# Performance work log

Hardware: AMD Instinct MI355X
Metric: run time of the kernel (lower is better)

The kernel has to match this reference:

```python
import jax, jax.numpy as jnp
import numpy as np

N, D_IN, D, E, B = 30000, 512, 512, 300000, 4096
N_RES, N_DNN = 2, 2
EPS = 1e-5


def _ln(x, g, b):
    mu = jnp.mean(x, axis=-1, keepdims=True)
    var = jnp.mean((x - mu) ** 2, axis=-1, keepdims=True)
    return (x - mu) * jax.lax.rsqrt(var + EPS) * g + b


def setup_inputs() -> dict:
    key = jax.random.key(0)
    ks = jax.random.split(key, 16)
    s = 1.0 / np.sqrt(D)
    inp = {
        "node_feat": jax.random.normal(ks[0], (N, D_IN), jnp.float32),
        "edge_hop0": jax.random.randint(ks[1], (2, E), 0, N, jnp.int32),
        "edge_hop1": jax.random.randint(ks[2], (2, E), 0, N, jnp.int32),
        "target_idx": jax.random.randint(ks[3], (B,), 0, N, jnp.int32),
        # node transform
        "Wt": jax.random.normal(ks[4], (D_IN, D), jnp.float32) / np.sqrt(D_IN),
        "bt": jnp.zeros((D,), jnp.float32),
        # GATConv (shared across both hops, one relation)
        "Wf": jax.random.normal(ks[5], (D, D), jnp.float32) * s,
        "bf": jnp.zeros((D,), jnp.float32),
        "w_att": jax.random.normal(ks[6], (2 * D,), jnp.float32) * s,
        "b_att": jnp.zeros((), jnp.float32),
        "gat_bias": jnp.zeros((D,), jnp.float32),
        # Res_DNN
        "Wp": jax.random.normal(ks[7], (D, D), jnp.float32) * s,
        "bp": jnp.zeros((D,), jnp.float32),
        "dnn_W": jax.random.normal(ks[8], (N_RES, N_DNN, D, D), jnp.float32) * s,
        "dnn_b": jnp.zeros((N_RES, N_DNN, D), jnp.float32),
        "dnn_g": jnp.ones((N_RES, N_DNN, D), jnp.float32),
        "dnn_beta": jnp.zeros((N_RES, N_DNN, D), jnp.float32),
        "res_g": jnp.ones((N_RES, D), jnp.float32),
        "res_beta": jnp.zeros((N_RES, D), jnp.float32),
        "Wc": jax.random.normal(ks[9], (D, 1), jnp.float32) * s,
        "bc": jnp.zeros((1,), jnp.float32),
    }
    return inp


def _gat(feat, edges, Wf, bf, w_att, b_att, gat_bias):
    # dst and src are the same node set / same features here
    h = feat @ Wf + bf                      # [N, D]
    di, si = edges[0], edges[1]             # [E], [E]
    # att(concat(dst_h, src_h)) == dst_h @ w[:D] + src_h @ w[D:] + b
    sd = h @ w_att[:D]                      # [N]
    ss = h @ w_att[D:]                      # [N]
    e = jnp.tanh(sd[di] + ss[si] + b_att)   # [E]
    # sparse softmax per destination row
    m = jax.ops.segment_max(e, di, num_segments=N)
    a = jnp.exp(e - m[di])
    denom = jax.ops.segment_sum(a, di, num_segments=N)
    alpha = a / denom[di]                   # [E]
    # sparse-mm aggregation
    out = jax.ops.segment_sum(alpha[:, None] * h[si], di, num_segments=N)
    return out + gat_bias


def reference(node_feat, edge_hop0, edge_hop1, target_idx, Wt, bt, Wf, bf,
              w_att, b_att, gat_bias, Wp, bp, dnn_W, dnn_b, dnn_g, dnn_beta,
              res_g, res_beta, Wc, bc):
    # node-type feature transform (dropout is identity at inference)
    feat = node_feat @ Wt + bt              # [N, D]
    # hops processed from last to first: hop1 then hop0
    for edges in (edge_hop1, edge_hop0):
        g = _gat(feat, edges, Wf, bf, w_att, b_att, gat_bias)
        feat = (feat + g) * 0.5             # mean of stacked [orig, gat_out]
    h = feat[target_idx]                    # [B, D]
    # Res_DNN head
    h = h @ Wp + bp
    for r in range(N_RES):
        sc = h
        for i in range(N_DNN):
            h = _ln(jnp.tanh(h @ dnn_W[r, i] + dnn_b[r, i]), dnn_g[r, i], dnn_beta[r, i])
        h = _ln(jnp.tanh(sc + h), res_g[r], res_beta[r])
    logits = h @ Wc + bc                    # [B, 1]
    return jax.nn.sigmoid(logits)
```

## Files before the change

### kernel.cpp

```cpp
#include <hip/hip_runtime.h>

#define D 512
typedef unsigned short ushort_t;
typedef __attribute__((ext_vector_type(8))) short bf16x8;
typedef __attribute__((ext_vector_type(4))) float f32x4;

static __device__ __forceinline__ ushort_t f2bf(float f) {
  unsigned u = __float_as_uint(f);
  u += 0x7fffu + ((u >> 16) & 1u);
  return (ushort_t)(u >> 16);
}
static __device__ __forceinline__ float bf2f(ushort_t h) {
  return __uint_as_float(((unsigned)h) << 16);
}

static __device__ __forceinline__ void gld_lds16(const void* g, void* lds) {
  __builtin_amdgcn_global_load_lds(
      (const __attribute__((address_space(1))) unsigned int*)g,
      (__attribute__((address_space(3))) unsigned int*)lds, 16, 0, 0);
}

__global__ __launch_bounds__(256) void pack_weight(
    const float* __restrict__ W, ushort_t* __restrict__ out, int K, int N, int nmat) {
  int i = blockIdx.x * 256 + threadIdx.x;
  const int per = K * N;
  if (i >= per * nmat) return;
  const int mat = i / per;
  const int r = i - mat * per;
  const int k = r / N, n = r - k * N;
  const int nt = n >> 4, col = n & 15, kt = k >> 5, kg = (k >> 3) & 3, j = k & 7;
  out[(size_t)mat * per + (((size_t)nt * (K >> 5) + kt) << 9) + ((kg << 4) + col) * 8 + j] =
      f2bf(W[(size_t)mat * per + r]);
}

__global__ __launch_bounds__(256) void conv_bf16_pad(
    const float* __restrict__ in, ushort_t* __restrict__ out, int M, int Mp, int K) {
  const size_t i4 = ((size_t)blockIdx.x * 256 + threadIdx.x) * 4;
  if (i4 >= (size_t)Mp * K) return;
  const int row = (int)(i4 / K);
  ushort4 o;
  if (row < M) {
    const float4 v = *reinterpret_cast<const float4*>(&in[i4]);
    o.x = f2bf(v.x); o.y = f2bf(v.y); o.z = f2bf(v.z); o.w = f2bf(v.w);
  } else {
    o.x = o.y = o.z = o.w = 0;
  }
  *reinterpret_cast<ushort4*>(&out[i4]) = o;
}

__global__ __launch_bounds__(256) void gemm_mfma(
    const ushort_t* __restrict__ A, const ushort_t* __restrict__ Bp,
    const float* __restrict__ bias, ushort_t* __restrict__ C16, int N, int K) {
  __shared__ __align__(16) ushort_t As[8 * 512];
  __shared__ __align__(16) ushort_t Bs[8 * 512];
  const int nwg = gridDim.x;
  const int q = nwg >> 3, rm = nwg & 7;
  const int xcd = blockIdx.x & 7, kk = blockIdx.x >> 3;
  const int lin = (xcd < rm ? xcd * (q + 1) : rm * (q + 1) + (xcd - rm) * q) + kk;
  const int m0 = (lin >> 2) * 128;
  const int n0 = (lin & 3) * 128;
  const int tid = threadIdx.x;
  const int lane = tid & 63;
  const int wid = tid >> 6;
  const int wm = wid >> 1, wn = wid & 1;
  const int arow = lane & 15;
  const int akoff = (lane >> 4) * 8;
  const int kt32 = K >> 5;
  f32x4 acc[4][4] = {};
  ushort_t* as0 = &As[(wid * 2 + 0) * 512];
  ushort_t* as1 = &As[(wid * 2 + 1) * 512];
  ushort_t* bs0 = &Bs[(wid * 2 + 0) * 512];
  ushort_t* bs1 = &Bs[(wid * 2 + 1) * 512];
  for (int k0 = 0; k0 < K; k0 += 32) {
    gld_lds16(&A[(size_t)(m0 + (wid * 2 + 0) * 16 + arow) * K + k0 + akoff], as0);
    gld_lds16(&A[(size_t)(m0 + (wid * 2 + 1) * 16 + arow) * K + k0 + akoff], as1);
    gld_lds16(&Bp[(((size_t)(n0 / 16 + wid * 2 + 0) * kt32 + (k0 >> 5)) << 9) + lane * 8], bs0);
    gld_lds16(&Bp[(((size_t)(n0 / 16 + wid * 2 + 1) * kt32 + (k0 >> 5)) << 9) + lane * 8], bs1);
    __syncthreads();
    bf16x8 af[4], bfr[4];
#pragma unroll
    for (int mi = 0; mi < 4; ++mi)
      af[mi] = *reinterpret_cast<const bf16x8*>(&As[(wm * 4 + mi) * 512 + lane * 8]);
#pragma unroll
    for (int ni = 0; ni < 4; ++ni)
      bfr[ni] = *reinterpret_cast<const bf16x8*>(&Bs[(wn * 4 + ni) * 512 + lane * 8]);
#pragma unroll
    for (int mi = 0; mi < 4; ++mi)
#pragma unroll
      for (int ni = 0; ni < 4; ++ni)
        acc[mi][ni] = __builtin_amdgcn_mfma_f32_16x16x32_bf16(af[mi], bfr[ni], acc[mi][ni], 0, 0, 0);
    __syncthreads();
  }
#pragma unroll
  for (int mi = 0; mi < 4; ++mi) {
    const int row = m0 + wm * 64 + mi * 16 + ((lane >> 4) << 2);
#pragma unroll
    for (int ni = 0; ni < 4; ++ni) {
      const int col = n0 + wn * 64 + ni * 16 + (lane & 15);
      const float bv = bias[col];
#pragma unroll
      for (int r = 0; r < 4; ++r)
        C16[(size_t)(row + r) * N + col] = f2bf(acc[mi][ni][r] + bv);
    }
  }
}

__global__ __launch_bounds__(256) void rowdot2_w(
    const ushort_t* __restrict__ hb, const float* __restrict__ w_att,
    float* __restrict__ sd, float* __restrict__ ss, int Nn) {
  const int r = blockIdx.x * 4 + (threadIdx.x >> 6);
  const int lane = threadIdx.x & 63;
  if (r >= Nn) return;
  const bf16x8 hv = *reinterpret_cast<const bf16x8*>(&hb[(size_t)r * D + lane * 8]);
  float d0 = 0.f, d1 = 0.f;
#pragma unroll
  for (int q = 0; q < 8; ++q) {
    const float v = bf2f((ushort_t)hv[q]);
    d0 += v * w_att[lane * 8 + q];
    d1 += v * w_att[D + lane * 8 + q];
  }
#pragma unroll
  for (int off = 32; off > 0; off >>= 1) {
    d0 += __shfl_xor(d0, off);
    d1 += __shfl_xor(d1, off);
  }
  if (lane == 0) { sd[r] = d0; ss[r] = d1; }
}

__global__ void count_deg2(const int* __restrict__ e1, const int* __restrict__ e0,
                           int* __restrict__ deg, int Nn, int E) {
  const int e = blockIdx.x * blockDim.x + threadIdx.x;
  if (e < E) {
    atomicAdd(&deg[e1[e]], 1);
    atomicAdd(&deg[Nn + e0[e]], 1);
  }
}

__global__ __launch_bounds__(256) void scan_block(
    const int* __restrict__ deg, int* __restrict__ incl, int* __restrict__ bsum, int n) {
  __shared__ int buf[256];
  const int t = threadIdx.x;
  const int i = blockIdx.x * 256 + t;
  const int v = (i < n) ? deg[i] : 0;
  buf[t] = v;
  __syncthreads();
  for (int off = 1; off < 256; off <<= 1) {
    const int y = (t >= off) ? buf[t - off] : 0;
    __syncthreads();
    buf[t] += y;
    __syncthreads();
  }
  if (i < n) incl[i] = buf[t];
  if (t == 255) bsum[blockIdx.x] = buf[255];
}

__global__ __launch_bounds__(256) void scan_sums(
    int* __restrict__ bsum, int nb, int* __restrict__ row_total) {
  __shared__ int buf[256];
  const int t = threadIdx.x;
  const int v = (t < nb) ? bsum[t] : 0;
  buf[t] = v;
  __syncthreads();
  for (int off = 1; off < 256; off <<= 1) {
    const int y = (t >= off) ? buf[t - off] : 0;
    __syncthreads();
    buf[t] += y;
    __syncthreads();
  }
  if (t < nb) bsum[t] = buf[t] - v;
  if (t == 0) *row_total = buf[255];
}

__global__ __launch_bounds__(256) void scan_finalize(
    const int* __restrict__ incl, const int* __restrict__ deg,
    const int* __restrict__ bsum, int* __restrict__ row_start,
    int* __restrict__ cursor, int n) {
  const int i = blockIdx.x * 256 + threadIdx.x;
  if (i >= n) return;
  const int v = incl[i] - deg[i] + bsum[i >> 8];
  row_start[i] = v;
  cursor[i] = v;
}

__global__ void fill_csr2(const int* __restrict__ e1, const int* __restrict__ e0,
                          int* __restrict__ cursor, int* __restrict__ csr_s,
                          int Nn, int E) {
  const int e = blockIdx.x * blockDim.x + threadIdx.x;
  if (e >= E) return;
  const int d1 = e1[e];
  csr_s[atomicAdd(&cursor[d1], 1)] = e1[E + e];
  const int d0 = e0[e];
  csr_s[atomicAdd(&cursor[Nn + d0], 1)] = e0[E + e];
}

__global__ __launch_bounds__(256) void gat_aggregate_w(
    ushort_t* __restrict__ featb, const ushort_t* __restrict__ hb,
    const float* __restrict__ sd, const float* __restrict__ ss,
    float* __restrict__ edge_e, const float* __restrict__ b_att_p,
    const float* __restrict__ gat_bias, const int* __restrict__ row_start,
    const int* __restrict__ csr_src, int Nn) {
  const int dst = blockIdx.x * 4 + (threadIdx.x >> 6);
  const int lane = threadIdx.x & 63;
  if (dst >= Nn) return;
  const int beg = row_start[dst];
  const int end = row_start[dst + 1];
  const int deg = end - beg;
  const float sdd = sd[dst];
  const float ba = b_att_p[0];
  float acc[8] = {};
  float inv;
  if (deg <= 64) {
    const int j0 = beg + lane;
    const bool valid = j0 < end;
    const float e = valid ? tanhf(sdd + ss[csr_src[j0]] + ba) : -1e30f;
    float m = e;
#pragma unroll
    for (int off = 32; off > 0; off >>= 1) m = fmaxf(m, __shfl_xor(m, off));
    float a = valid ? expf(e - m) : 0.f;
    float s = a;
#pragma unroll
    for (int off = 32; off > 0; off >>= 1) s += __shfl_xor(s, off);
    inv = (s > 0.f) ? 1.f / s : 0.f;
    int k = 0;
    for (; k + 1 < deg; k += 2) {
      const float w0 = __shfl(a, k) * inv;
      const float w1 = __shfl(a, k + 1) * inv;
      const int s0 = csr_src[beg + k];
      const int s1 = csr_src[beg + k + 1];
      const bf16x8 h0 = *reinterpret_cast<const bf16x8*>(&hb[(size_t)s0 * D + lane * 8]);
      const bf16x8 h1 = *reinterpret_cast<const bf16x8*>(&hb[(size_t)s1 * D + lane * 8]);
#pragma unroll
      for (int q = 0; q < 8; ++q)
        acc[q] += w0 * bf2f((ushort_t)h0[q]) + w1 * bf2f((ushort_t)h1[q]);
    }
    if (k < deg) {
      const float w = __shfl(a, k) * inv;
      const int s0 = csr_src[beg + k];
      const bf16x8 h0 = *reinterpret_cast<const bf16x8*>(&hb[(size_t)s0 * D + lane * 8]);
#pragma unroll
      for (int q = 0; q < 8; ++q) acc[q] += w * bf2f((ushort_t)h0[q]);
    }
  } else {
    float m = -1e30f;
    for (int j = beg + lane; j < end; j += 64) {
      const float e = tanhf(sdd + ss[csr_src[j]] + ba);
      edge_e[j] = e;
      m = fmaxf(m, e);
    }
#pragma unroll
    for (int off = 32; off > 0; off >>= 1) m = fmaxf(m, __shfl_xor(m, off));
    asm volatile("s_waitcnt vmcnt(0)" ::: "memory");
    float s = 0.f;
    for (int j = beg + lane; j < end; j += 64) {
      const float a2 = expf(edge_e[j] - m);
      edge_e[j] = a2;
      s += a2;
    }
#pragma unroll
    for (int off = 32; off > 0; off >>= 1) s += __shfl_xor(s, off);
    asm volatile("s_waitcnt vmcnt(0)" ::: "memory");
    inv = (s > 0.f) ? 1.f / s : 0.f;
    for (int j = beg; j < end; ++j) {
      const float w = edge_e[j] * inv;
      const int sidx = csr_src[j];
      const bf16x8 hv = *reinterpret_cast<const bf16x8*>(&hb[(size_t)sidx * D + lane * 8]);
#pragma unroll
      for (int q = 0; q < 8; ++q) acc[q] += w * bf2f((ushort_t)hv[q]);
    }
  }
  const size_t o = (size_t)dst * D + lane * 8;
  bf16x8 fv = *reinterpret_cast<const bf16x8*>(&featb[o]);
#pragma unroll
  for (int q = 0; q < 8; ++q) {
    const float f = (bf2f((ushort_t)fv[q]) + acc[q] + gat_bias[lane * 8 + q]) * 0.5f;
    fv[q] = (short)f2bf(f);
  }
  *reinterpret_cast<bf16x8*>(&featb[o]) = fv;
}

__global__ __launch_bounds__(1024, 4) void head_fused(
    const ushort_t* __restrict__ featb, const int* __restrict__ tidx,
    const ushort_t* __restrict__ pWp, const float* __restrict__ bp,
    const ushort_t* __restrict__ pDW, const float* __restrict__ dnn_b,
    const float* __restrict__ dnn_g, const float* __restrict__ dnn_be,
    const float* __restrict__ res_g, const float* __restrict__ res_be,
    const float* __restrict__ Wc, const float* __restrict__ bc,
    float* __restrict__ out) {
  __shared__ __align__(16) ushort_t A_lds[16 * 512];
  __shared__ float lsum[16][16], lsq[16][16], meanv[16], rsv[16];
  const int tid = threadIdx.x;
  const int lane = tid & 63;
  const int wave = tid >> 6;
  const int nt0 = wave * 2;
  const int c15 = lane & 15;
  const int rgrp = lane >> 4;

  {
    const int row = tid >> 6, col8 = tid & 63;
    const int g = tidx[blockIdx.x * 16 + row];
    const bf16x8 v = *reinterpret_cast<const bf16x8*>(&featb[(size_t)g * D + col8 * 8]);
    *reinterpret_cast<bf16x8*>(&A_lds[row * 512 + (col8 ^ (row & 7)) * 8]) = v;
  }
  __syncthreads();

  auto do_gemm = [&](const ushort_t* __restrict__ W, f32x4& a0, f32x4& a1) {
    a0 = f32x4{0.f, 0.f, 0.f, 0.f};
    a1 = f32x4{0.f, 0.f, 0.f, 0.f};
    bf16x8 c0 = *reinterpret_cast<const bf16x8*>(
        &W[(((size_t)nt0 * 16 + 0) << 9) + lane * 8]);
    bf16x8 c1 = *reinterpret_cast<const bf16x8*>(
        &W[(((size_t)(nt0 + 1) * 16 + 0) << 9) + lane * 8]);
#pragma unroll
    for (int kt = 0; kt < 16; ++kt) {
      bf16x8 n0 = c0, n1 = c1;
      if (kt < 15) {
        n0 = *reinterpret_cast<const bf16x8*>(
            &W[(((size_t)nt0 * 16 + kt + 1) << 9) + lane * 8]);
        n1 = *reinterpret_cast<const bf16x8*>(
            &W[(((size_t)(nt0 + 1) * 16 + kt + 1) << 9) + lane * 8]);
      }
      const int col8 = kt * 4 + rgrp;
      const bf16x8 af = *reinterpret_cast<const bf16x8*>(
          &A_lds[c15 * 512 + (col8 ^ (c15 & 7)) * 8]);
      a0 = __builtin_amdgcn_mfma_f32_16x16x32_bf16(af, c0, a0, 0, 0, 0);
      a1 = __builtin_amdgcn_mfma_f32_16x16x32_bf16(af, c1, a1, 0, 0, 0);
      c0 = n0;
      c1 = n1;
    }
  };

  auto block_ln = [&](f32x4& v0, f32x4& v1, const float* __restrict__ g,
                      const float* __restrict__ be) {
    float psum[4], psq[4];
#pragma unroll
    for (int r = 0; r < 4; ++r) {
      psum[r] = v0[r] + v1[r];
      psq[r] = v0[r] * v0[r] + v1[r] * v1[r];
    }
#pragma unroll
    for (int off = 8; off > 0; off >>= 1)
#pragma unroll
      for (int r = 0; r < 4; ++r) {
        psum[r] += __shfl_xor(psum[r], off);
        psq[r] += __shfl_xor(psq[r], off);
      }
    if (c15 == 0) {
#pragma unroll
      for (int r = 0; r < 4; ++r) {
        lsum[wave][rgrp * 4 + r] = psum[r];
        lsq[wave][rgrp * 4 + r] = psq[r];
      }
    }
    __syncthreads();
    if (tid < 16) {
      float s = 0.f, qq = 0.f;
#pragma unroll
      for (int w = 0; w < 16; ++w) { s += lsum[w][tid]; qq += lsq[w][tid]; }
      const float mean = s * (1.f / 512.f);
      const float var = qq * (1.f / 512.f) - mean * mean;
      meanv[tid] = mean;
      rsv[tid] = rsqrtf(var + 1e-5f);
    }
    __syncthreads();
    const int col0 = nt0 * 16 + c15;
    const int col1 = (nt0 + 1) * 16 + c15;
    const float g0 = g[col0], b0 = be[col0];
    const float g1 = g[col1], b1 = be[col1];
#pragma unroll
    for (int r = 0; r < 4; ++r) {
      const int row = rgrp * 4 + r;
      v0[r] = (v0[r] - meanv[row]) * rsv[row] * g0 + b0;
      v1[r] = (v1[r] - meanv[row]) * rsv[row] * g1 + b1;
    }
  };

  auto store_A = [&](const f32x4& v0, const f32x4& v1) {
    const int col0 = nt0 * 16 + c15;
    const int col1 = (nt0 + 1) * 16 + c15;
#pragma unroll
    for (int r = 0; r < 4; ++r) {
      const int row = rgrp * 4 + r;
      A_lds[row * 512 + (((col0 >> 3) ^ (row & 7)) << 3) + (col0 & 7)] = f2bf(v0[r]);
      A_lds[row * 512 + (((col1 >> 3) ^ (row & 7)) << 3) + (col1 & 7)] = f2bf(v1[r]);
    }
  };

  f32x4 sc0, sc1, acc0, acc1, ln0, ln1;

  do_gemm(pWp, acc0, acc1);
  {
    const float bv0 = bp[nt0 * 16 + c15];
    const float bv1 = bp[(nt0 + 1) * 16 + c15];
#pragma unroll
    for (int r = 0; r < 4; ++r) { sc0[r] = acc0[r] + bv0; sc1[r] = acc1[r] + bv1; }
  }
  __syncthreads();
  store_A(sc0, sc1);
  __syncthreads();

  for (int rb = 0; rb < 2; ++rb) {
    {
      const int st = rb * 2;
      do_gemm(pDW + (size_t)st * D * D, acc0, acc1);
      const float bv0 = dnn_b[st * D + nt0 * 16 + c15];
      const float bv1 = dnn_b[st * D + (nt0 + 1) * 16 + c15];
#pragma unroll
      for (int r = 0; r < 4; ++r) {
        acc0[r] = tanhf(acc0[r] + bv0);
        acc1[r] = tanhf(acc1[r] + bv1);
      }
      block_ln(acc0, acc1, dnn_g + st * D, dnn_be + st * D);
      store_A(acc0, acc1);
      __syncthreads();
    }
    {
      const int st = rb * 2 + 1;
      do_gemm(pDW + (size_t)st * D * D, ln0, ln1);
      const float bv0 = dnn_b[st * D + nt0 * 16 + c15];
      const float bv1 = dnn_b[st * D + (nt0 + 1) * 16 + c15];
#pragma unroll
      for (int r = 0; r < 4; ++r) {
        ln0[r] = tanhf(ln0[r] + bv0);
        ln1[r] = tanhf(ln1[r] + bv1);
      }
      block_ln(ln0, ln1, dnn_g + st * D, dnn_be + st * D);
    }
#pragma unroll
    for (int r = 0; r < 4; ++r) {
      acc0[r] = tanhf(sc0[r] + ln0[r]);
      acc1[r] = tanhf(sc1[r] + ln1[r]);
    }
    block_ln(acc0, acc1, res_g + rb * D, res_be + rb * D);
    sc0 = acc0;
    sc1 = acc1;
    if (rb == 0) {
      store_A(sc0, sc1);
      __syncthreads();
    }
  }

  float pr[4];
  {
    const float w0 = Wc[nt0 * 16 + c15];
    const float w1 = Wc[(nt0 + 1) * 16 + c15];
#pragma unroll
    for (int r = 0; r < 4; ++r) pr[r] = sc0[r] * w0 + sc1[r] * w1;
  }
#pragma unroll
  for (int off = 8; off > 0; off >>= 1)
#pragma unroll
    for (int r = 0; r < 4; ++r) pr[r] += __shfl_xor(pr[r], off);
  __syncthreads();
  if (c15 == 0) {
#pragma unroll
    for (int r = 0; r < 4; ++r) lsum[wave][rgrp * 4 + r] = pr[r];
  }
  __syncthreads();
  if (tid < 16) {
    float s = 0.f;
#pragma unroll
    for (int w = 0; w < 16; ++w) s += lsum[w][tid];
    out[blockIdx.x * 16 + tid] = 1.f / (1.f + expf(-(s + bc[0])));
  }
}

extern "C" void kernel_launch(void* const* d_in, const int* in_sizes, int n_in,
                              void* d_out, int out_size, void* d_ws, size_t ws_size,
                              hipStream_t stream) {
  (void)n_in; (void)out_size; (void)ws_size;
  const float* node_feat = (const float*)d_in[0];
  const int* edge0 = (const int*)d_in[1];
  const int* edge1 = (const int*)d_in[2];
  const int* tidx = (const int*)d_in[3];
  const float* Wt = (const float*)d_in[4];
  const float* bt = (const float*)d_in[5];
  const float* Wf = (const float*)d_in[6];
  const float* bfp = (const float*)d_in[7];
  const float* w_att = (const float*)d_in[8];
  const float* b_att = (const float*)d_in[9];
  const float* gat_bias = (const float*)d_in[10];
  const float* Wp = (const float*)d_in[11];
  const float* bp = (const float*)d_in[12];
  const float* dnn_W = (const float*)d_in[13];
  const float* dnn_b = (const float*)d_in[14];
  const float* dnn_g = (const float*)d_in[15];
  const float* dnn_be = (const float*)d_in[16];
  const float* res_g = (const float*)d_in[17];
  const float* res_be = (const float*)d_in[18];
  const float* Wc = (const float*)d_in[19];
  const float* bc = (const float*)d_in[20];
  float* out = (float*)d_out;

  const int Nn = in_sizes[0] / D;
  const int E = in_sizes[1] / 2;
  const int B = in_sizes[3];
  const int K_IN = in_sizes[4] / D;
  const int Mp = (Nn + 127) / 128 * 128;
  const int N2 = 2 * Nn;

  char* p = (char*)d_ws;
  auto alloc = [&](size_t bytes) -> char* {
    char* r = p;
    p += (bytes + 255) & ~(size_t)255;
    return r;
  };
  ushort_t* featb = (ushort_t*)alloc((size_t)Mp * D * 2);
  ushort_t* hb = (ushort_t*)alloc((size_t)Mp * D * 2);
  float* sd = (float*)alloc((size_t)Nn * 4);
  float* ss = (float*)alloc((size_t)Nn * 4);
  int* deg = (int*)alloc((size_t)N2 * 4);
  int* incl = (int*)alloc((size_t)N2 * 4);
  int* bsum = (int*)alloc(256 * 4);
  int* cursor = (int*)alloc((size_t)N2 * 4);
  int* row_start = (int*)alloc((size_t)(N2 + 1) * 4);
  int* csr_s = (int*)alloc((size_t)2 * E * 4);
  float* edge_e = (float*)alloc((size_t)2 * E * 4);
  ushort_t* pWt = (ushort_t*)alloc((size_t)K_IN * D * 2);
  ushort_t* pWf = (ushort_t*)alloc((size_t)D * D * 2);
  ushort_t* pWp = (ushort_t*)alloc((size_t)D * D * 2);
  ushort_t* pDWall = (ushort_t*)alloc((size_t)4 * D * D * 2);

  dim3 blk(256);
  const int nb2 = (N2 + 255) / 256;
  const int nw4 = (Nn + 3) / 4;

  {
    pack_weight<<<(K_IN * D + 255) / 256, blk, 0, stream>>>(Wt, pWt, K_IN, D, 1);
    pack_weight<<<(D * D + 255) / 256, blk, 0, stream>>>(Wf, pWf, D, D, 1);
    pack_weight<<<(D * D + 255) / 256, blk, 0, stream>>>(Wp, pWp, D, D, 1);
    pack_weight<<<(4 * D * D + 255) / 256, blk, 0, stream>>>(dnn_W, pDWall, D, D, 4);
    conv_bf16_pad<<<((size_t)Mp * K_IN / 4 + 255) / 256, blk, 0, stream>>>(
        node_feat, hb , Nn, Mp, K_IN);
  }

  hipMemsetAsync(deg, 0, (size_t)N2 * 4, stream);
  count_deg2<<<(E + 255) / 256, blk, 0, stream>>>(edge1, edge0, deg, Nn, E);
  scan_block<<<nb2, blk, 0, stream>>>(deg, incl, bsum, N2);
  scan_sums<<<1, blk, 0, stream>>>(bsum, nb2, &row_start[N2]);
  scan_finalize<<<nb2, blk, 0, stream>>>(incl, deg, bsum, row_start, cursor, N2);
  fill_csr2<<<(E + 255) / 256, blk, 0, stream>>>(edge1, edge0, cursor, csr_s, Nn, E);

  gemm_mfma<<<dim3(4 * (Mp / 128)), blk, 0, stream>>>(hb, pWt, bt, featb, D, K_IN);

  for (int hp = 0; hp < 2; ++hp) {
    gemm_mfma<<<dim3(4 * (Mp / 128)), blk, 0, stream>>>(featb, pWf, bfp, hb, D, D);
    rowdot2_w<<<nw4, blk, 0, stream>>>(hb, w_att, sd, ss, Nn);
    gat_aggregate_w<<<nw4, blk, 0, stream>>>(featb, hb, sd, ss, edge_e, b_att,
                                             gat_bias, row_start + hp * Nn, csr_s, Nn);
  }

  head_fused<<<B / 16, dim3(1024), 0, stream>>>(
      featb, tidx, pWp, bp, pDWall, dnn_b, dnn_g, dnn_be, res_g, res_be,
      Wc, bc, out);
}
```

Measured before the change: 357.8 us.

## Double-buffer GEMM LDS tiles and unroll GAT gather with shuffled indices

The GEMM now double-buffers its A/B LDS tiles, issuing the next k-slice's global-to-LDS loads before the MFMAs on the current slice. This drops one barrier per iteration and overlaps load latency with compute. The GAT aggregation for small-degree rows now broadcasts source indices and pre-normalized weights via lane shuffles instead of re-reading csr_src, unrolls the gather by four to keep more row loads in flight, and hoists the feature load to the top of the kernel. These add LDS usage and register pressure, which may lower occupancy.

After: 355.4 us. About the same (-0.7%).

```diff
diff --git a/kernel.cpp b/kernel.cpp
--- a/kernel.cpp
+++ b/kernel.cpp
@@ -51,8 +51,8 @@
 __global__ __launch_bounds__(256) void gemm_mfma(
     const ushort_t* __restrict__ A, const ushort_t* __restrict__ Bp,
     const float* __restrict__ bias, ushort_t* __restrict__ C16, int N, int K) {
-  __shared__ __align__(16) ushort_t As[8 * 512];
-  __shared__ __align__(16) ushort_t Bs[8 * 512];
+  __shared__ __align__(16) ushort_t As[2][8 * 512];
+  __shared__ __align__(16) ushort_t Bs[2][8 * 512];
   const int nwg = gridDim.x;
   const int q = nwg >> 3, rm = nwg & 7;
   const int xcd = blockIdx.x & 7, kk = blockIdx.x >> 3;
@@ -67,29 +67,38 @@
   const int akoff = (lane >> 4) * 8;
   const int kt32 = K >> 5;
   f32x4 acc[4][4] = {};
-  ushort_t* as0 = &As[(wid * 2 + 0) * 512];
-  ushort_t* as1 = &As[(wid * 2 + 1) * 512];
-  ushort_t* bs0 = &Bs[(wid * 2 + 0) * 512];
-  ushort_t* bs1 = &Bs[(wid * 2 + 1) * 512];
-  for (int k0 = 0; k0 < K; k0 += 32) {
-    gld_lds16(&A[(size_t)(m0 + (wid * 2 + 0) * 16 + arow) * K + k0 + akoff], as0);
-    gld_lds16(&A[(size_t)(m0 + (wid * 2 + 1) * 16 + arow) * K + k0 + akoff], as1);
-    gld_lds16(&Bp[(((size_t)(n0 / 16 + wid * 2 + 0) * kt32 + (k0 >> 5)) << 9) + lane * 8], bs0);
-    gld_lds16(&Bp[(((size_t)(n0 / 16 + wid * 2 + 1) * kt32 + (k0 >> 5)) << 9) + lane * 8], bs1);
-    __syncthreads();
+
+  auto stage = [&](int kt, int b) {
+    const int k0 = kt * 32;
+    gld_lds16(&A[(size_t)(m0 + (wid * 2 + 0) * 16 + arow) * K + k0 + akoff],
+              &As[b][(wid * 2 + 0) * 512]);
+    gld_lds16(&A[(size_t)(m0 + (wid * 2 + 1) * 16 + arow) * K + k0 + akoff],
+              &As[b][(wid * 2 + 1) * 512]);
+    gld_lds16(&Bp[(((size_t)(n0 / 16 + wid * 2 + 0) * kt32 + kt) << 9) + lane * 8],
+              &Bs[b][(wid * 2 + 0) * 512]);
+    gld_lds16(&Bp[(((size_t)(n0 / 16 + wid * 2 + 1) * kt32 + kt) << 9) + lane * 8],
+              &Bs[b][(wid * 2 + 1) * 512]);
+  };
+
+  stage(0, 0);
+  __syncthreads();
+  int cur = 0;
+  for (int t = 0; t < kt32; ++t) {
+    if (t + 1 < kt32) stage(t + 1, cur ^ 1);
     bf16x8 af[4], bfr[4];
 #pragma unroll
     for (int mi = 0; mi < 4; ++mi)
-      af[mi] = *reinterpret_cast<const bf16x8*>(&As[(wm * 4 + mi) * 512 + lane * 8]);
+      af[mi] = *reinterpret_cast<const bf16x8*>(&As[cur][(wm * 4 + mi) * 512 + lane * 8]);
 #pragma unroll
     for (int ni = 0; ni < 4; ++ni)
-      bfr[ni] = *reinterpret_cast<const bf16x8*>(&Bs[(wn * 4 + ni) * 512 + lane * 8]);
+      bfr[ni] = *reinterpret_cast<const bf16x8*>(&Bs[cur][(wn * 4 + ni) * 512 + lane * 8]);
 #pragma unroll
     for (int mi = 0; mi < 4; ++mi)
 #pragma unroll
       for (int ni = 0; ni < 4; ++ni)
         acc[mi][ni] = __builtin_amdgcn_mfma_f32_16x16x32_bf16(af[mi], bfr[ni], acc[mi][ni], 0, 0, 0);
     __syncthreads();
+    cur ^= 1;
   }
 #pragma unroll
   for (int mi = 0; mi < 4; ++mi) {
@@ -207,38 +216,43 @@
   const int deg = end - beg;
   const float sdd = sd[dst];
   const float ba = b_att_p[0];
+  const size_t o = (size_t)dst * D + lane * 8;
+  bf16x8 fv = *reinterpret_cast<const bf16x8*>(&featb[o]);
   float acc[8] = {};
-  float inv;
   if (deg <= 64) {
     const int j0 = beg + lane;
     const bool valid = j0 < end;
-    const float e = valid ? tanhf(sdd + ss[csr_src[j0]] + ba) : -1e30f;
+    const int slane = valid ? csr_src[j0] : 0;
+    const float e = valid ? tanhf(sdd + ss[slane] + ba) : -1e30f;
     float m = e;
 #pragma unroll
     for (int off = 32; off > 0; off >>= 1) m = fmaxf(m, __shfl_xor(m, off));
-    float a = valid ? expf(e - m) : 0.f;
+    const float a = valid ? expf(e - m) : 0.f;
     float s = a;
 #pragma unroll
     for (int off = 32; off > 0; off >>= 1) s += __shfl_xor(s, off);
-    inv = (s > 0.f) ? 1.f / s : 0.f;
+    const float w = a * ((s > 0.f) ? 1.f / s : 0.f);
     int k = 0;
-    for (; k + 1 < deg; k += 2) {
-      const float w0 = __shfl(a, k) * inv;
-      const float w1 = __shfl(a, k + 1) * inv;
-      const int s0 = csr_src[beg + k];
-      const int s1 = csr_src[beg + k + 1];
+    for (; k + 3 < deg; k += 4) {
+      const float w0 = __shfl(w, k), w1 = __shfl(w, k + 1);
+      const float w2 = __shfl(w, k + 2), w3 = __shfl(w, k + 3);
+      const int s0 = __shfl(slane, k), s1 = __shfl(slane, k + 1);
+      const int s2 = __shfl(slane, k + 2), s3 = __shfl(slane, k + 3);
       const bf16x8 h0 = *reinterpret_cast<const bf16x8*>(&hb[(size_t)s0 * D + lane * 8]);
       const bf16x8 h1 = *reinterpret_cast<const bf16x8*>(&hb[(size_t)s1 * D + lane * 8]);
-#pragma unroll
-      for (int q = 0; q < 8; ++q)
-        acc[q] += w0 * bf2f((ushort_t)h0[q]) + w1 * bf2f((ushort_t)h1[q]);
-    }
-    if (k < deg) {
-      const float w = __shfl(a, k) * inv;
-      const int s0 = csr_src[beg + k];
-      const bf16x8 h0 = *reinterpret_cast<const bf16x8*>(&hb[(size_t)s0 * D + lane * 8]);
-#pragma unroll
-      for (int q = 0; q < 8; ++q) acc[q] += w * bf2f((ushort_t)h0[q]);
+      const bf16x8 h2 = *reinterpret_cast<const bf16x8*>(&hb[(size_t)s2 * D + lane * 8]);
+      const bf16x8 h3 = *reinterpret_cast<const bf16x8*>(&hb[(size_t)s3 * D + lane * 8]);
+#pragma unroll
+      for (int qq = 0; qq < 8; ++qq)
+        acc[qq] += w0 * bf2f((ushort_t)h0[qq]) + w1 * bf2f((ushort_t)h1[qq]) +
+                   w2 * bf2f((ushort_t)h2[qq]) + w3 * bf2f((ushort_t)h3[qq]);
+    }
+    for (; k < deg; ++k) {
+      const float wk = __shfl(w, k);
+      const int sk = __shfl(slane, k);
+      const bf16x8 h0 = *reinterpret_cast<const bf16x8*>(&hb[(size_t)sk * D + lane * 8]);
+#pragma unroll
+      for (int qq = 0; qq < 8; ++qq) acc[qq] += wk * bf2f((ushort_t)h0[qq]);
     }
   } else {
     float m = -1e30f;
@@ -259,17 +273,15 @@
 #pragma unroll
     for (int off = 32; off > 0; off >>= 1) s += __shfl_xor(s, off);
     asm volatile("s_waitcnt vmcnt(0)" ::: "memory");
-    inv = (s > 0.f) ? 1.f / s : 0.f;
+    const float inv = (s > 0.f) ? 1.f / s : 0.f;
     for (int j = beg; j < end; ++j) {
       const float w = edge_e[j] * inv;
       const int sidx = csr_src[j];
       const bf16x8 hv = *reinterpret_cast<const bf16x8*>(&hb[(size_t)sidx * D + lane * 8]);
 #pragma unroll
-      for (int q = 0; q < 8; ++q) acc[q] += w * bf2f((ushort_t)hv[q]);
-    }
-  }
-  const size_t o = (size_t)dst * D + lane * 8;
-  bf16x8 fv = *reinterpret_cast<const bf16x8*>(&featb[o]);
+      for (int qq = 0; qq < 8; ++qq) acc[qq] += w * bf2f((ushort_t)hv[qq]);
+    }
+  }
 #pragma unroll
   for (int q = 0; q < 8; ++q) {
     const float f = (bf2f((ushort_t)fv[q]) + acc[q] + gat_bias[lane * 8 + q]) * 0.5f;
```
